# Kernel optimization log

Measured on AMD Instinct MI355X. Metric: run time of the kernel, lower is better.

Reference implementation:

```python
import jax, jax.numpy as jnp
import numpy as np

B, T, H, N = 4, 2048, 1024, 16
DT_MIN, DT_MAX = 1e-3, 1e-1
A_INIT_MIN, A_INIT_MAX = 0.5, 2.0


def _inv_softplus(x):
    # log(exp(x) - 1), numerically stable
    return x + jnp.log(-jnp.expm1(-x))


def setup_inputs() -> dict:
    key = jax.random.key(0)
    kx, ka, kb, kc, kw, kdt = jax.random.split(key, 6)
    x = jax.random.normal(kx, (B, T, H), dtype=jnp.float32)
    A_log = jax.random.uniform(ka, (H, N), minval=np.log(A_INIT_MIN), maxval=np.log(A_INIT_MAX), dtype=jnp.float32)
    B_mat = 0.02 * jax.random.normal(kb, (H, N), dtype=jnp.float32)
    C_mat = 0.02 * jax.random.normal(kc, (H, N), dtype=jnp.float32)
    D_vec = jnp.ones((H,), dtype=jnp.float32)
    W_dt = 0.02 * jax.random.normal(kw, (H, H), dtype=jnp.float32)
    b_dt = _inv_softplus(jax.random.uniform(kdt, (H,), minval=DT_MIN, maxval=DT_MAX, dtype=jnp.float32))
    return {"x": x, "A_log": A_log, "B_mat": B_mat, "C_mat": C_mat, "D_vec": D_vec, "W_dt": W_dt, "b_dt": b_dt}


def reference(x, A_log, B_mat, C_mat, D_vec, W_dt, b_dt):
    # in_proj is Identity since input_size == hidden_size
    u = x  # (B, T, H)
    A = -jnp.exp(A_log)  # (H, N)
    # dt for all timesteps at once: softplus(u @ W_dt^T + b_dt) -> (B, T, H)
    dt = jax.nn.softplus(jnp.einsum('bth,gh->btg', u, W_dt) + b_dt)
    state0 = jnp.zeros((u.shape[0], A_log.shape[0], A_log.shape[1]), dtype=u.dtype)

    def step(state, inp):
        dt_t, u_t = inp  # (B, H), (B, H)
        dtA = dt_t[..., None]  # (B, H, 1)
        A_bar = jnp.exp(dtA * A)                       # (B, H, N)
        state = A_bar * state + (dtA * B_mat) * u_t[..., None]
        y_t = jnp.einsum('bhn,hn->bh', state, C_mat) + D_vec * u_t
        return state, y_t

    # scan over time axis
    state_final, ys = jax.lax.scan(step, state0, (dt.transpose(1, 0, 2), u.transpose(1, 0, 2)))
    out = ys.transpose(1, 0, 2)  # (B, T, H)
    return out, state_final
```

## Files before the change

kernel.cpp:

```cpp
#include <hip/hip_runtime.h>
#include <stdint.h>

#define BB 4
#define TT 2048
#define HH 1024
#define NN 16
#define KK 1024
#define GG 1024
#define MM (BB*TT)
#define NCHUNK 64
#define TC (TT/NCHUNK)
#define HB 256

#if __has_builtin(__builtin_amdgcn_exp2f)
#define FAST_EXP2(x) __builtin_amdgcn_exp2f(x)
#else
#define FAST_EXP2(x) __expf((x) * 0.6931471805599453f)
#endif
#define EXPSCALE 1.4426950408889634f

typedef __attribute__((ext_vector_type(8))) short short8;
typedef __attribute__((ext_vector_type(4))) float f32x4;

__device__ __forceinline__ unsigned short f2bf(float f) {
  union { float f; unsigned u; } a; a.f = f;
  unsigned u = a.u;
  u += 0x7fffu + ((u >> 16) & 1u);
  return (unsigned short)(u >> 16);
}

__device__ __forceinline__ unsigned pack_half2(float a, float b) {
  union { _Float16 h[2]; unsigned u; } p;
  p.h[0] = (_Float16)a; p.h[1] = (_Float16)b;
  return p.u;
}

__global__ __launch_bounds__(256) void cvt2_f32_bf16(const float* __restrict__ srcA,
                                                     unsigned short* __restrict__ dstA, int n4a,
                                                     const float* __restrict__ srcB,
                                                     unsigned short* __restrict__ dstB, int n4b) {
  int i = blockIdx.x * blockDim.x + threadIdx.x;
  const float* s; unsigned short* d; int j;
  if (i < n4a) { s = srcA; d = dstA; j = i; }
  else         { s = srcB; d = dstB; j = i - n4a; if (j >= n4b) return; }
  float4 a = ((const float4*)s)[j];
  ushort4 o;
  o.x = f2bf(a.x); o.y = f2bf(a.y); o.z = f2bf(a.z); o.w = f2bf(a.w);
  ((ushort4*)d)[j] = o;
}

__global__ __launch_bounds__(256) void gemm_dt(const unsigned short* __restrict__ xb,
                                               const unsigned short* __restrict__ wb,
                                               const float* __restrict__ b_dt,
                                               _Float16* __restrict__ dtH) {
  __shared__ short lsA[128 * 32];
  __shared__ short lsB[128 * 32];
  const int tid  = threadIdx.x;
  const int w    = tid >> 6;
  const int lane = tid & 63;
  const int bid  = blockIdx.x;
  const int swz  = (bid & 7) * 64 + (bid >> 3);
  const int m0 = (swz >> 3) * 128;
  const int g0 = (swz & 7) * 128;

  const int ea  = w * 1024 + lane * 8;
  const int am0 = ea >> 5,         ak0 = ea & 31;
  const int am1 = (ea + 512) >> 5, ak1 = (ea + 512) & 31;
  const unsigned short* gA0 = xb + (size_t)(m0 + am0) * KK + ak0;
  const unsigned short* gA1 = xb + (size_t)(m0 + am1) * KK + ak1;
  const unsigned short* gB0 = wb + (size_t)(g0 + am0) * KK + ak0;
  const unsigned short* gB1 = wb + (size_t)(g0 + am1) * KK + ak1;
  short* lA0 = lsA + w * 1024;
  short* lB0 = lsB + w * 1024;

  const int wm   = (w >> 1) * 64;
  const int wn   = (w & 1) * 64;
  const int lrow = lane & 15;
  const int lq   = lane >> 4;

  f32x4 acc[4][4];
  const f32x4 zero = {0.f, 0.f, 0.f, 0.f};
#pragma unroll
  for (int i = 0; i < 4; ++i)
#pragma unroll
    for (int j = 0; j < 4; ++j) acc[i][j] = zero;

  for (int kt = 0; kt < KK / 32; ++kt) {
    const int ko = kt * 32;
    __builtin_amdgcn_global_load_lds((__attribute__((address_space(1))) void*)(gA0 + ko),
                                     (__attribute__((address_space(3))) void*)(lA0), 16, 0, 0);
    __builtin_amdgcn_global_load_lds((__attribute__((address_space(1))) void*)(gA1 + ko),
                                     (__attribute__((address_space(3))) void*)(lA0 + 512), 16, 0, 0);
    __builtin_amdgcn_global_load_lds((__attribute__((address_space(1))) void*)(gB0 + ko),
                                     (__attribute__((address_space(3))) void*)(lB0), 16, 0, 0);
    __builtin_amdgcn_global_load_lds((__attribute__((address_space(1))) void*)(gB1 + ko),
                                     (__attribute__((address_space(3))) void*)(lB0 + 512), 16, 0, 0);
    __syncthreads();

    short8 af[4], bfr[4];
#pragma unroll
    for (int mi = 0; mi < 4; ++mi)
      af[mi] = *(const short8*)&lsA[(wm + mi * 16 + lrow) * 32 + lq * 8];
#pragma unroll
    for (int ni = 0; ni < 4; ++ni)
      bfr[ni] = *(const short8*)&lsB[(wn + ni * 16 + lrow) * 32 + lq * 8];
#pragma unroll
    for (int mi = 0; mi < 4; ++mi)
#pragma unroll
      for (int ni = 0; ni < 4; ++ni)
        acc[mi][ni] = __builtin_amdgcn_mfma_f32_16x16x32_bf16(af[mi], bfr[ni], acc[mi][ni], 0, 0, 0);
    __syncthreads();
  }

  const int mrow = m0 + wm + lq * 4;
#pragma unroll
  for (int ni = 0; ni < 4; ++ni) {
    const int g = g0 + wn + ni * 16 + lrow;
    const float bias = b_dt[g];
#pragma unroll
    for (int mi = 0; mi < 4; ++mi)
#pragma unroll
      for (int r = 0; r < 4; ++r) {
        float z = acc[mi][ni][r] + bias;
        dtH[(size_t)(mrow + mi * 16 + r) * GG + g] =
            (_Float16)(fmaxf(z, 0.f) + __logf(1.f + __expf(-fabsf(z))));
      }
  }
}

__global__ __launch_bounds__(256, 4) void ssm_phase1(const float* __restrict__ x,
                                                     const _Float16* __restrict__ dtH,
                                                     const float* __restrict__ A_log,
                                                     const float* __restrict__ Bm_,
                                                     const float* __restrict__ Cm_,
                                                     const float* __restrict__ Dv_,
                                                     float* __restrict__ sloc,
                                                     float* __restrict__ sdArr,
                                                     unsigned* __restrict__ ylsd) {
  const int tid = threadIdx.x;
  const int bid = blockIdx.x;
  const int hb = bid & (HH / HB - 1);
  const int b  = (bid >> 2) & (BB - 1);
  const int c  = bid >> 4;
  const int h  = hb * HB + tid;

  const size_t base = ((size_t)b * TT + c * TC) * HH + h;
  const float*    up = x + base;
  const _Float16* dp = dtH + base;
  unsigned*       yp = ylsd + base;

  float Ae[NN], Cb[NN];
#pragma unroll
  for (int n = 0; n < NN; ++n) {
    Ae[n] = -__expf(A_log[h * NN + n]) * EXPSCALE;
    Cb[n] = Cm_[h * NN + n] * Bm_[h * NN + n];
  }
  const float Dv = Dv_[h];

  float s[NN];
#pragma unroll
  for (int n = 0; n < NN; ++n) s[n] = 0.f;
  float sd = 0.f;

#pragma unroll
  for (int j = 0; j < TC / 8; ++j) {
    float uu[8], dv[8];
#pragma unroll
    for (int i = 0; i < 8; ++i) {
      uu[i] = up[(size_t)(j * 8 + i) * HH];
      dv[i] = (float)dp[(size_t)(j * 8 + i) * HH];
    }
#pragma unroll
    for (int i = 0; i < 8; ++i) {
      const float dtv = dv[i];
      const float uv  = uu[i];
      const float du  = dtv * uv;
      sd += dtv;
      float y0 = Dv * uv, y1 = 0.f, y2 = 0.f, y3 = 0.f;
#pragma unroll
      for (int n = 0; n < NN; n += 4) {
        float ab;
        ab = FAST_EXP2(dtv * Ae[n]);     s[n]     = fmaf(ab, s[n],     du); y0 = fmaf(Cb[n],     s[n],     y0);
        ab = FAST_EXP2(dtv * Ae[n + 1]); s[n + 1] = fmaf(ab, s[n + 1], du); y1 = fmaf(Cb[n + 1], s[n + 1], y1);
        ab = FAST_EXP2(dtv * Ae[n + 2]); s[n + 2] = fmaf(ab, s[n + 2], du); y2 = fmaf(Cb[n + 2], s[n + 2], y2);
        ab = FAST_EXP2(dtv * Ae[n + 3]); s[n + 3] = fmaf(ab, s[n + 3], du); y3 = fmaf(Cb[n + 3], s[n + 3], y3);
      }
      yp[(size_t)(j * 8 + i) * HH] = pack_half2((y0 + y1) + (y2 + y3), sd);
    }
  }

  float* sp = sloc + (((size_t)c * BB + b) * HH + h) * NN;
#pragma unroll
  for (int n = 0; n < NN; n += 4) {
    f32x4 v = {s[n], s[n + 1], s[n + 2], s[n + 3]};
    *(f32x4*)&sp[n] = v;
  }
  sdArr[((size_t)c * BB + b) * HH + h] = sd;
}

__global__ __launch_bounds__(256) void ssm_phase2(float* __restrict__ sloc,
                                                  const float* __restrict__ sdArr,
                                                  const float* __restrict__ A_log,
                                                  const float* __restrict__ Bm_,
                                                  float* __restrict__ stateOut) {
  const int id = blockIdx.x * 256 + threadIdx.x;
  const int hn = id & (HH * NN - 1);
  const int bh = id >> 4;
  const float Ae = -__expf(A_log[hn]) * EXPSCALE;
  float carry = 0.f;
#pragma unroll 4
  for (int ch = 0; ch < NCHUNK; ++ch) {
    const size_t idx = (size_t)ch * (BB * HH * NN) + id;
    const float sl = sloc[idx];
    const float dc = FAST_EXP2(Ae * sdArr[(size_t)ch * (BB * HH) + bh]);
    sloc[idx] = carry;
    carry = fmaf(dc, carry, sl);
  }
  stateOut[id] = Bm_[hn] * carry;
}

__global__ __launch_bounds__(256, 4) void ssm_phase3(const unsigned* __restrict__ ylsd,
                                                     const float* __restrict__ A_log,
                                                     const float* __restrict__ Bm_,
                                                     const float* __restrict__ Cm_,
                                                     const float* __restrict__ carryBuf,
                                                     float* __restrict__ out) {
  const int tid = threadIdx.x;
  const int bid = blockIdx.x;
  const int hb = bid & (HH / HB - 1);
  const int b  = (bid >> 2) & (BB - 1);
  const int c  = bid >> 4;
  const int h  = hb * HB + tid;

  const size_t base = ((size_t)b * TT + c * TC) * HH + h;
  const unsigned* yp = ylsd + base;
  float*          yo = out + base;

  float Ae[NN], cc[NN];
#pragma unroll
  for (int n = 0; n < NN; ++n) Ae[n] = -__expf(A_log[h * NN + n]) * EXPSCALE;

  const float* cp = carryBuf + (((size_t)c * BB + b) * HH + h) * NN;
#pragma unroll
  for (int n = 0; n < NN; n += 4) {
    f32x4 v = *(const f32x4*)&cp[n];
#pragma unroll
    for (int q = 0; q < 4; ++q)
      cc[n + q] = Cm_[h * NN + n + q] * Bm_[h * NN + n + q] * v[q];
  }

#pragma unroll
  for (int j = 0; j < TC / 8; ++j) {
    unsigned vv[8];
#pragma unroll
    for (int i = 0; i < 8; ++i) vv[i] = yp[(size_t)(j * 8 + i) * HH];
#pragma unroll
    for (int i = 0; i < 8; ++i) {
      union { unsigned u; _Float16 hh[2]; } q; q.u = vv[i];
      const float sdv = (float)q.hh[1];
      float y0 = (float)q.hh[0], y1 = 0.f, y2 = 0.f, y3 = 0.f;
#pragma unroll
      for (int n = 0; n < NN; n += 4) {
        y0 = fmaf(cc[n],     FAST_EXP2(Ae[n]     * sdv), y0);
        y1 = fmaf(cc[n + 1], FAST_EXP2(Ae[n + 1] * sdv), y1);
        y2 = fmaf(cc[n + 2], FAST_EXP2(Ae[n + 2] * sdv), y2);
        y3 = fmaf(cc[n + 3], FAST_EXP2(Ae[n + 3] * sdv), y3);
      }
      yo[(size_t)(j * 8 + i) * HH] = (y0 + y1) + (y2 + y3);
    }
  }
}

extern "C" void kernel_launch(void* const* d_in, const int* in_sizes, int n_in,
                              void* d_out, int out_size, void* d_ws, size_t ws_size,
                              hipStream_t stream) {
  const float* x     = (const float*)d_in[0];
  const float* A_log = (const float*)d_in[1];
  const float* B_mat = (const float*)d_in[2];
  const float* C_mat = (const float*)d_in[3];
  const float* D_vec = (const float*)d_in[4];
  const float* W_dt  = (const float*)d_in[5];
  const float* b_dt  = (const float*)d_in[6];
  float* out = (float*)d_out;

  char* ws = (char*)d_ws;
  unsigned short* xb   = (unsigned short*)(ws);
  unsigned short* wb   = (unsigned short*)(ws + 16777216);
  _Float16*       dtH  = (_Float16*)(ws + 18874368);
  unsigned*       ylsd = (unsigned*)(ws + 35651584);
  float*          sloc  = (float*)(ws);
  float*          sdArr = (float*)(ws + 16777216);
  float* stateOut = out + (size_t)BB * TT * HH;

  const int n4x = MM * KK / 4, n4w = GG * KK / 4;
  cvt2_f32_bf16<<<(n4x + n4w + 255) / 256, 256, 0, stream>>>(x, xb, n4x, W_dt, wb, n4w);
  gemm_dt<<<(MM / 128) * (GG / 128), 256, 0, stream>>>(xb, wb, b_dt, dtH);

  const int nblk = (HH / HB) * BB * NCHUNK;
  ssm_phase1<<<nblk, 256, 0, stream>>>(x, dtH, A_log, B_mat, C_mat, D_vec, sloc, sdArr, ylsd);
  ssm_phase2<<<(BB * HH * NN) / 256, 256, 0, stream>>>(sloc, sdArr, A_log, B_mat, stateOut);
  ssm_phase3<<<nblk, 256, 0, stream>>>(ylsd, A_log, B_mat, C_mat, sloc, out);
}
```

Measured before the change: 189.1 us.

## Retile dt GEMM to 128x64 with K=64 and double-buffer loads in scan phases

The dt GEMM moves from 128x128 tiles with K-step 32 to 128x64 tiles with K-step 64. That doubles the grid to 1024 blocks, halves the barriers per unit of K, and adds an occupancy hint of 4 blocks per SM. Phases 1 and 3 now load the next 8 timesteps while the current 8 are being computed, to hide global load latency. The costs are more registers for the ping-pong buffers, and more A-tile reloads in the GEMM because the N tile is smaller.

```diff
diff --git a/kernel.cpp b/kernel.cpp
--- a/kernel.cpp
+++ b/kernel.cpp
@@ -49,73 +49,97 @@
   ((ushort4*)d)[j] = o;
 }
 
-__global__ __launch_bounds__(256) void gemm_dt(const unsigned short* __restrict__ xb,
-                                               const unsigned short* __restrict__ wb,
-                                               const float* __restrict__ b_dt,
-                                               _Float16* __restrict__ dtH) {
-  __shared__ short lsA[128 * 32];
-  __shared__ short lsB[128 * 32];
+__global__ __launch_bounds__(256, 4) void gemm_dt(const unsigned short* __restrict__ xb,
+                                                  const unsigned short* __restrict__ wb,
+                                                  const float* __restrict__ b_dt,
+                                                  _Float16* __restrict__ dtH) {
+  __shared__ short lsA[128 * 64];
+  __shared__ short lsB[64 * 64];
   const int tid  = threadIdx.x;
   const int w    = tid >> 6;
   const int lane = tid & 63;
   const int bid  = blockIdx.x;
-  const int swz  = (bid & 7) * 64 + (bid >> 3);
-  const int m0 = (swz >> 3) * 128;
-  const int g0 = (swz & 7) * 128;
-
-  const int ea  = w * 1024 + lane * 8;
-  const int am0 = ea >> 5,         ak0 = ea & 31;
-  const int am1 = (ea + 512) >> 5, ak1 = (ea + 512) & 31;
-  const unsigned short* gA0 = xb + (size_t)(m0 + am0) * KK + ak0;
-  const unsigned short* gA1 = xb + (size_t)(m0 + am1) * KK + ak1;
-  const unsigned short* gB0 = wb + (size_t)(g0 + am0) * KK + ak0;
-  const unsigned short* gB1 = wb + (size_t)(g0 + am1) * KK + ak1;
-  short* lA0 = lsA + w * 1024;
-  short* lB0 = lsB + w * 1024;
+  const int swz  = (bid & 7) * 128 + (bid >> 3);
+  const int m0 = (swz >> 4) * 128;
+  const int g0 = (swz & 15) * 64;
+
+  const int r8 = lane >> 3;
+  const int c8 = (lane & 7) * 8;
+  const unsigned short* gA[4];
+  short*                lA[4];
+#pragma unroll
+  for (int q = 0; q < 4; ++q) {
+    const int row = w * 32 + q * 8 + r8;
+    gA[q] = xb + (size_t)(m0 + row) * KK + c8;
+    lA[q] = lsA + row * 64;
+  }
+  const unsigned short* gB[2];
+  short*                lB[2];
+#pragma unroll
+  for (int q = 0; q < 2; ++q) {
+    const int row = w * 16 + q * 8 + r8;
+    gB[q] = wb + (size_t)(g0 + row) * KK + c8;
+    lB[q] = lsB + row * 64;
+  }
 
   const int wm   = (w >> 1) * 64;
-  const int wn   = (w & 1) * 64;
+  const int wg   = (w & 1) * 32;
   const int lrow = lane & 15;
   const int lq   = lane >> 4;
 
-  f32x4 acc[4][4];
+  int aoff[4][2], boff[2][2];
+#pragma unroll
+  for (int mi = 0; mi < 4; ++mi) {
+    const int row = wm + mi * 16 + lrow;
+    aoff[mi][0] = row * 64 + lq * 8;
+    aoff[mi][1] = row * 64 + 32 + lq * 8;
+  }
+#pragma unroll
+  for (int ni = 0; ni < 2; ++ni) {
+    const int row = wg + ni * 16 + lrow;
+    boff[ni][0] = row * 64 + lq * 8;
+    boff[ni][1] = row * 64 + 32 + lq * 8;
+  }
+
+  f32x4 acc[4][2];
   const f32x4 zero = {0.f, 0.f, 0.f, 0.f};
 #pragma unroll
   for (int i = 0; i < 4; ++i)
 #pragma unroll
-    for (int j = 0; j < 4; ++j) acc[i][j] = zero;
-
-  for (int kt = 0; kt < KK / 32; ++kt) {
-    const int ko = kt * 32;
-    __builtin_amdgcn_global_load_lds((__attribute__((address_space(1))) void*)(gA0 + ko),
-                                     (__attribute__((address_space(3))) void*)(lA0), 16, 0, 0);
-    __builtin_amdgcn_global_load_lds((__attribute__((address_space(1))) void*)(gA1 + ko),
-                                     (__attribute__((address_space(3))) void*)(lA0 + 512), 16, 0, 0);
-    __builtin_amdgcn_global_load_lds((__attribute__((address_space(1))) void*)(gB0 + ko),
-                                     (__attribute__((address_space(3))) void*)(lB0), 16, 0, 0);
-    __builtin_amdgcn_global_load_lds((__attribute__((address_space(1))) void*)(gB1 + ko),
-                                     (__attribute__((address_space(3))) void*)(lB0 + 512), 16, 0, 0);
+    for (int j = 0; j < 2; ++j) acc[i][j] = zero;
+
+  for (int kt = 0; kt < KK / 64; ++kt) {
+    const int ko = kt * 64;
+#pragma unroll
+    for (int q = 0; q < 4; ++q)
+      __builtin_amdgcn_global_load_lds((__attribute__((address_space(1))) void*)(gA[q] + ko),
+                                       (__attribute__((address_space(3))) void*)(lA[q]), 16, 0, 0);
+#pragma unroll
+    for (int q = 0; q < 2; ++q)
+      __builtin_amdgcn_global_load_lds((__attribute__((address_space(1))) void*)(gB[q] + ko),
+                                       (__attribute__((address_space(3))) void*)(lB[q]), 16, 0, 0);
     __syncthreads();
 
-    short8 af[4], bfr[4];
-#pragma unroll
-    for (int mi = 0; mi < 4; ++mi)
-      af[mi] = *(const short8*)&lsA[(wm + mi * 16 + lrow) * 32 + lq * 8];
-#pragma unroll
-    for (int ni = 0; ni < 4; ++ni)
-      bfr[ni] = *(const short8*)&lsB[(wn + ni * 16 + lrow) * 32 + lq * 8];
-#pragma unroll
-    for (int mi = 0; mi < 4; ++mi)
-#pragma unroll
-      for (int ni = 0; ni < 4; ++ni)
-        acc[mi][ni] = __builtin_amdgcn_mfma_f32_16x16x32_bf16(af[mi], bfr[ni], acc[mi][ni], 0, 0, 0);
+#pragma unroll
+    for (int kk = 0; kk < 2; ++kk) {
+      short8 af[4], bfr[2];
+#pragma unroll
+      for (int mi = 0; mi < 4; ++mi) af[mi] = *(const short8*)&lsA[aoff[mi][kk]];
+#pragma unroll
+      for (int ni = 0; ni < 2; ++ni) bfr[ni] = *(const short8*)&lsB[boff[ni][kk]];
+#pragma unroll
+      for (int mi = 0; mi < 4; ++mi)
+#pragma unroll
+        for (int ni = 0; ni < 2; ++ni)
+          acc[mi][ni] = __builtin_amdgcn_mfma_f32_16x16x32_bf16(af[mi], bfr[ni], acc[mi][ni], 0, 0, 0);
+    }
     __syncthreads();
   }
 
   const int mrow = m0 + wm + lq * 4;
 #pragma unroll
-  for (int ni = 0; ni < 4; ++ni) {
-    const int g = g0 + wn + ni * 16 + lrow;
+  for (int ni = 0; ni < 2; ++ni) {
+    const int g = g0 + wg + ni * 16 + lrow;
     const float bias = b_dt[g];
 #pragma unroll
     for (int mi = 0; mi < 4; ++mi)
@@ -125,6 +149,39 @@
         dtH[(size_t)(mrow + mi * 16 + r) * GG + g] =
             (_Float16)(fmaxf(z, 0.f) + __logf(1.f + __expf(-fabsf(z))));
       }
+  }
+}
+
+__device__ __forceinline__ void p1_load8(const float* __restrict__ up,
+                                         const _Float16* __restrict__ dp, int t0,
+                                         float (&U)[8], _Float16 (&D)[8]) {
+#pragma unroll
+  for (int i = 0; i < 8; ++i) {
+    U[i] = up[(size_t)(t0 + i) * HH];
+    D[i] = dp[(size_t)(t0 + i) * HH];
+  }
+}
+
+__device__ __forceinline__ void p1_comp8(const float (&U)[8], const _Float16 (&D)[8], int t0,
+                                         float (&s)[NN], float& sd,
+                                         const float (&Ae)[NN], const float (&Cb)[NN],
+                                         float Dv, unsigned* __restrict__ yp) {
+#pragma unroll
+  for (int i = 0; i < 8; ++i) {
+    const float dtv = (float)D[i];
+    const float uv  = U[i];
+    const float du  = dtv * uv;
+    sd += dtv;
+    float y0 = Dv * uv, y1 = 0.f, y2 = 0.f, y3 = 0.f;
+#pragma unroll
+    for (int n = 0; n < NN; n += 4) {
+      float ab;
+      ab = FAST_EXP2(dtv * Ae[n]);     s[n]     = fmaf(ab, s[n],     du); y0 = fmaf(Cb[n],     s[n],     y0);
+      ab = FAST_EXP2(dtv * Ae[n + 1]); s[n + 1] = fmaf(ab, s[n + 1], du); y1 = fmaf(Cb[n + 1], s[n + 1], y1);
+      ab = FAST_EXP2(dtv * Ae[n + 2]); s[n + 2] = fmaf(ab, s[n + 2], du); y2 = fmaf(Cb[n + 2], s[n + 2], y2);
+      ab = FAST_EXP2(dtv * Ae[n + 3]); s[n + 3] = fmaf(ab, s[n + 3], du); y3 = fmaf(Cb[n + 3], s[n + 3], y3);
+    }
+    yp[(size_t)(t0 + i) * HH] = pack_half2((y0 + y1) + (y2 + y3), sd);
   }
 }
 
@@ -162,32 +219,16 @@
   for (int n = 0; n < NN; ++n) s[n] = 0.f;
   float sd = 0.f;
 
-#pragma unroll
-  for (int j = 0; j < TC / 8; ++j) {
-    float uu[8], dv[8];
-#pragma unroll
-    for (int i = 0; i < 8; ++i) {
-      uu[i] = up[(size_t)(j * 8 + i) * HH];
-      dv[i] = (float)dp[(size_t)(j * 8 + i) * HH];
-    }
-#pragma unroll
-    for (int i = 0; i < 8; ++i) {
-      const float dtv = dv[i];
-      const float uv  = uu[i];
-      const float du  = dtv * uv;
-      sd += dtv;
-      float y0 = Dv * uv, y1 = 0.f, y2 = 0.f, y3 = 0.f;
-#pragma unroll
-      for (int n = 0; n < NN; n += 4) {
-        float ab;
-        ab = FAST_EXP2(dtv * Ae[n]);     s[n]     = fmaf(ab, s[n],     du); y0 = fmaf(Cb[n],     s[n],     y0);
-        ab = FAST_EXP2(dtv * Ae[n + 1]); s[n + 1] = fmaf(ab, s[n + 1], du); y1 = fmaf(Cb[n + 1], s[n + 1], y1);
-        ab = FAST_EXP2(dtv * Ae[n + 2]); s[n + 2] = fmaf(ab, s[n + 2], du); y2 = fmaf(Cb[n + 2], s[n + 2], y2);
-        ab = FAST_EXP2(dtv * Ae[n + 3]); s[n + 3] = fmaf(ab, s[n + 3], du); y3 = fmaf(Cb[n + 3], s[n + 3], y3);
-      }
-      yp[(size_t)(j * 8 + i) * HH] = pack_half2((y0 + y1) + (y2 + y3), sd);
-    }
-  }
+  float Ua[8], Ub[8];
+  _Float16 Da[8], Db[8];
+  p1_load8(up, dp, 0, Ua, Da);
+  p1_load8(up, dp, 8, Ub, Db);
+  p1_comp8(Ua, Da, 0, s, sd, Ae, Cb, Dv, yp);
+  p1_load8(up, dp, 16, Ua, Da);
+  p1_comp8(Ub, Db, 8, s, sd, Ae, Cb, Dv, yp);
+  p1_load8(up, dp, 24, Ub, Db);
+  p1_comp8(Ua, Da, 16, s, sd, Ae, Cb, Dv, yp);
+  p1_comp8(Ub, Db, 24, s, sd, Ae, Cb, Dv, yp);
 
   float* sp = sloc + (((size_t)c * BB + b) * HH + h) * NN;
 #pragma unroll
@@ -219,6 +260,31 @@
   stateOut[id] = Bm_[hn] * carry;
 }
 
+__device__ __forceinline__ void p3_load8(const unsigned* __restrict__ yp, int t0,
+                                         unsigned (&V)[8]) {
+#pragma unroll
+  for (int i = 0; i < 8; ++i) V[i] = yp[(size_t)(t0 + i) * HH];
+}
+
+__device__ __forceinline__ void p3_comp8(const unsigned (&V)[8], int t0,
+                                         const float (&Ae)[NN], const float (&cc)[NN],
+                                         float* __restrict__ yo) {
+#pragma unroll
+  for (int i = 0; i < 8; ++i) {
+    union { unsigned u; _Float16 hh[2]; } q; q.u = V[i];
+    const float sdv = (float)q.hh[1];
+    float y0 = (float)q.hh[0], y1 = 0.f, y2 = 0.f, y3 = 0.f;
+#pragma unroll
+    for (int n = 0; n < NN; n += 4) {
+      y0 = fmaf(cc[n],     FAST_EXP2(Ae[n]     * sdv), y0);
+      y1 = fmaf(cc[n + 1], FAST_EXP2(Ae[n + 1] * sdv), y1);
+      y2 = fmaf(cc[n + 2], FAST_EXP2(Ae[n + 2] * sdv), y2);
+      y3 = fmaf(cc[n + 3], FAST_EXP2(Ae[n + 3] * sdv), y3);
+    }
+    yo[(size_t)(t0 + i) * HH] = (y0 + y1) + (y2 + y3);
+  }
+}
+
 __global__ __launch_bounds__(256, 4) void ssm_phase3(const unsigned* __restrict__ ylsd,
                                                      const float* __restrict__ A_log,
                                                      const float* __restrict__ Bm_,
@@ -249,26 +315,15 @@
       cc[n + q] = Cm_[h * NN + n + q] * Bm_[h * NN + n + q] * v[q];
   }
 
-#pragma unroll
-  for (int j = 0; j < TC / 8; ++j) {
-    unsigned vv[8];
-#pragma unroll
-    for (int i = 0; i < 8; ++i) vv[i] = yp[(size_t)(j * 8 + i) * HH];
-#pragma unroll
-    for (int i = 0; i < 8; ++i) {
-      union { unsigned u; _Float16 hh[2]; } q; q.u = vv[i];
-      const float sdv = (float)q.hh[1];
-      float y0 = (float)q.hh[0], y1 = 0.f, y2 = 0.f, y3 = 0.f;
-#pragma unroll
-      for (int n = 0; n < NN; n += 4) {
-        y0 = fmaf(cc[n],     FAST_EXP2(Ae[n]     * sdv), y0);
-        y1 = fmaf(cc[n + 1], FAST_EXP2(Ae[n + 1] * sdv), y1);
-        y2 = fmaf(cc[n + 2], FAST_EXP2(Ae[n + 2] * sdv), y2);
-        y3 = fmaf(cc[n + 3], FAST_EXP2(Ae[n + 3] * sdv), y3);
-      }
-      yo[(size_t)(j * 8 + i) * HH] = (y0 + y1) + (y2 + y3);
-    }
-  }
+  unsigned Va[8], Vb[8];
+  p3_load8(yp, 0, Va);
+  p3_load8(yp, 8, Vb);
+  p3_comp8(Va, 0, Ae, cc, yo);
+  p3_load8(yp, 16, Va);
+  p3_comp8(Vb, 8, Ae, cc, yo);
+  p3_load8(yp, 24, Vb);
+  p3_comp8(Va, 16, Ae, cc, yo);
+  p3_comp8(Vb, 24, Ae, cc, yo);
 }
 
 extern "C" void kernel_launch(void* const* d_in, const int* in_sizes, int n_in,
@@ -294,7 +349,7 @@
 
   const int n4x = MM * KK / 4, n4w = GG * KK / 4;
   cvt2_f32_bf16<<<(n4x + n4w + 255) / 256, 256, 0, stream>>>(x, xb, n4x, W_dt, wb, n4w);
-  gemm_dt<<<(MM / 128) * (GG / 128), 256, 0, stream>>>(xb, wb, b_dt, dtH);
+  gemm_dt<<<(MM / 128) * (GG / 64), 256, 0, stream>>>(xb, wb, b_dt, dtH);
 
   const int nblk = (HH / HB) * BB * NCHUNK;
   ssm_phase1<<<nblk, 256, 0, stream>>>(x, dtH, A_log, B_mat, C_mat, D_vec, sloc, sdArr, ylsd);
```

After: 191.7 us. Within noise of the previous version (+1.4%).
